# Kernel optimization log

Hardware: AMD Instinct MI355X
Metric: run time of the kernel (lower is better)

The kernel has to match this reference:

```python
import jax, jax.numpy as jnp
import numpy as np

X_DIM, Y_DIM = 16, 8
D_MODEL, N_HEADS, N_LAYERS = 256, 8, 8
D_HEAD = D_MODEL // N_HEADS            # 32 (hidden_out_size // n_heads)
D_FF = D_HEAD * 8 * N_HEADS            # 2048 (feed_forward_dimensions)
B, S_PAST, S_FUT = 4, 1024, 512
MIN_STD = 0.01
LN_EPS = 1e-5
ATTN_EPS = 1e-6


def setup_inputs() -> dict:
    key = jax.random.key(0)
    ks = jax.random.split(key, 24)
    def nrm(k, shape, s=0.02):
        return jax.random.normal(k, shape, jnp.float32) * s
    L, d, dff = N_LAYERS, D_MODEL, D_FF
    x_size = X_DIM + Y_DIM
    return {
        "past_x": jax.random.normal(ks[0], (B, S_PAST, X_DIM), jnp.float32),
        "past_y": jax.random.normal(ks[1], (B, S_PAST, Y_DIM), jnp.float32),
        "future_x": jax.random.normal(ks[2], (B, S_FUT, X_DIM), jnp.float32),
        "enc_W": nrm(ks[3], (x_size, d)), "enc_b": jnp.zeros((d,), jnp.float32),
        "Wq": nrm(ks[4], (L, d, d)), "bq": jnp.zeros((L, d), jnp.float32),
        "Wk": nrm(ks[5], (L, d, d)), "bk": jnp.zeros((L, d), jnp.float32),
        "Wv": nrm(ks[6], (L, d, d)), "bv": jnp.zeros((L, d), jnp.float32),
        "Wo": nrm(ks[7], (L, d, d)), "bo": jnp.zeros((L, d), jnp.float32),
        "ln1_w": jnp.ones((L, d), jnp.float32), "ln1_b": jnp.zeros((L, d), jnp.float32),
        "W1": nrm(ks[8], (L, d, dff)), "b1": jnp.zeros((L, dff), jnp.float32),
        "W2": nrm(ks[9], (L, dff, d)), "b2": jnp.zeros((L, d), jnp.float32),
        "ln2_w": jnp.ones((L, d), jnp.float32), "ln2_b": jnp.zeros((L, d), jnp.float32),
        "mean_W": nrm(ks[10], (d, Y_DIM)), "mean_b": jnp.zeros((Y_DIM,), jnp.float32),
        "std_W": nrm(ks[11], (d, Y_DIM)), "std_b": jnp.zeros((Y_DIM,), jnp.float32),
    }


def _ln(x, w, b):
    m = jnp.mean(x, axis=-1, keepdims=True)
    v = jnp.var(x, axis=-1, keepdims=True)
    return (x - m) * jax.lax.rsqrt(v + LN_EPS) * w + b


def _causal_linear_attn(q, k, v):
    # q,k,v: [B, N, H, D]; phi(x) = elu(x) + 1 (fast_transformers default feature map)
    q = jax.nn.elu(q) + 1.0
    k = jax.nn.elu(k) + 1.0
    # cumulative outer-product state S_i = sum_{j<=i} phi(k_j) v_j^T : [B,N,H,D,D]
    kv = jnp.cumsum(jnp.einsum('bnhd,bnhm->bnhdm', k, v), axis=1)
    num = jnp.einsum('bnhd,bnhdm->bnhm', q, kv)
    z = jnp.einsum('bnhd,bnhd->bnh', q, jnp.cumsum(k, axis=1))
    return num / (z[..., None] + ATTN_EPS)


def _forward(past_x, past_y, future_x, enc_W, enc_b, Wq, bq, Wk, bk, Wv, bv,
             Wo, bo, ln1_w, ln1_b, W1, b1, W2, b2, ln2_w, ln2_b,
             mean_W, mean_b, std_W, std_b):
    Bz, Sf = future_x.shape[0], future_x.shape[1]
    steps = past_y.shape[1]
    # future y placeholder = last observed y, repeated
    fy = jnp.repeat(past_y[:, -1:, :], Sf, axis=1)
    context = jnp.concatenate([past_x, past_y], axis=-1)
    target = jnp.concatenate([future_x, fy], axis=-1)
    x = jax.lax.stop_gradient(jnp.concatenate([context, target], axis=1))  # .detach()
    x = x @ enc_W + enc_b                      # [B, N, D_MODEL]
    N = x.shape[1]
    for i in range(N_LAYERS):
        q = (x @ Wq[i] + bq[i]).reshape(Bz, N, N_HEADS, D_HEAD)
        k = (x @ Wk[i] + bk[i]).reshape(Bz, N, N_HEADS, D_HEAD)
        v = (x @ Wv[i] + bv[i]).reshape(Bz, N, N_HEADS, D_HEAD)
        a = _causal_linear_attn(q, k, v).reshape(Bz, N, D_MODEL)
        x = _ln(x + (a @ Wo[i] + bo[i]), ln1_w[i], ln1_b[i])   # post-norm (fast_transformers)
        y = jax.nn.relu(x @ W1[i] + b1[i]) @ W2[i] + b2[i]
        x = _ln(x + y, ln2_w[i], ln2_b[i])
    out = x[:, steps:, :]                      # keep only the target segment
    mean = out @ mean_W + mean_b
    sigma = MIN_STD + (1.0 - MIN_STD) * jax.nn.softplus(out @ std_W + std_b)
    return mean, sigma


def reference(past_x, past_y, future_x, enc_W, enc_b, Wq, bq, Wk, bk, Wv, bv,
              Wo, bo, ln1_w, ln1_b, W1, b1, W2, b2, ln2_w, ln2_b,
              mean_W, mean_b, std_W, std_b):
    return _forward(past_x, past_y, future_x, enc_W, enc_b, Wq, bq, Wk, bk,
                    Wv, bv, Wo, bo, ln1_w, ln1_b, W1, b1, W2, b2,
                    ln2_w, ln2_b, mean_W, mean_b, std_W, std_b)
```

## Files before the change

kernel.cpp:

```cpp
#include <hip/hip_runtime.h>
#include <hip/hip_bf16.h>
#include <math.h>

#define BB 4
#define SP 1024
#define SF 512
#define NN 1536
#define DD 256
#define HH 8
#define DH 32
#define DFF 2048
#define LL 8
#define TOK (BB*NN)
#define NSEG 48
#define SEGLEN 32

typedef __attribute__((ext_vector_type(8))) short bf16x8;
typedef __attribute__((ext_vector_type(4))) float f32x4;
typedef __hip_bfloat16 bf16;

__device__ __forceinline__ void gld_lds16(const void* g, void* l) {
    __builtin_amdgcn_global_load_lds(
        (const __attribute__((address_space(1))) void*)g,
        (__attribute__((address_space(3))) void*)l, 16, 0, 0);
}

__device__ __forceinline__ unsigned short f2bf_u(float f) {
    return __builtin_bit_cast(unsigned short, __float2bfloat16(f));
}

__device__ __forceinline__ void wtrans_tile(
    const float* __restrict__ s, bf16* __restrict__ d, int K, int N,
    int k0, int n0)
{
    __shared__ float tile[64][65];
    int t = threadIdx.x, c = t & 63, r4 = t >> 6;
    #pragma unroll
    for (int rr = 0; rr < 64; rr += 4)
        tile[rr+r4][c] = s[(size_t)(k0+rr+r4)*N + n0 + c];
    __syncthreads();
    #pragma unroll
    for (int rr = 0; rr < 64; rr += 4) {
        int n = rr + r4;
        d[(size_t)(n0+n)*K + k0 + c] = __float2bfloat16(tile[c][n]);
    }
}

__global__ __launch_bounds__(256) void wtrans_kernel(
    const float* __restrict__ src, bf16* __restrict__ dst, int K, int N)
{
    wtrans_tile(src + (size_t)blockIdx.z*K*N, dst + (size_t)blockIdx.z*K*N,
                K, N, blockIdx.x*64, blockIdx.y*64);
}

__global__ __launch_bounds__(256) void wtrans4_kernel(
    const float* __restrict__ Wq, const float* __restrict__ Wk,
    const float* __restrict__ Wv, const float* __restrict__ Wo,
    bf16* __restrict__ Wqt, bf16* __restrict__ Wkt,
    bf16* __restrict__ Wvt, bf16* __restrict__ Wot)
{
    int z = blockIdx.z, which = z >> 3, l = z & 7;
    const float* s = (which == 0 ? Wq : which == 1 ? Wk : which == 2 ? Wv : Wo)
                     + (size_t)l*DD*DD;
    bf16* d = (which == 0 ? Wqt : which == 1 ? Wkt : which == 2 ? Wvt : Wot)
              + (size_t)l*DD*DD;
    wtrans_tile(s, d, DD, DD, blockIdx.x*64, blockIdx.y*64);
}

template<int BM, bool SLICE, bool BOUT>
__device__ __forceinline__ void gemm_core(
    const bf16* __restrict__ A, const bf16* __restrict__ Wt,
    const float* __restrict__ bias, float* __restrict__ Cf,
    bf16* __restrict__ Cb, int N, int K, int epi, int kc0, int kc1)
{
    constexpr int MI = BM/32;
    __shared__ bf16 As[BM*64];
    __shared__ bf16 Bs[128*64];
    int tid = threadIdx.x, lane = tid & 63, wid = tid >> 6;
    int m0 = blockIdx.x*BM, n0 = blockIdx.y*128;
    int wm = (wid & 1)*(BM/2), wn = (wid >> 1)*64;

    f32x4 acc[MI][4] = {};

    int rA = wid*(BM/4) + (lane >> 3);
    int rB = wid*32 + (lane >> 3);
    int c_st = (lane & 7)*8;
    const bf16* Ag = A  + (size_t)(m0 + rA)*K + c_st;
    const bf16* Bg = Wt + (size_t)(n0 + rB)*K + c_st;
    bf16* Asw = As + (wid*(BM/4))*64;
    bf16* Bsw = Bs + (wid*32)*64;

    int a_off = (wm + (lane & 15))*64 + (lane >> 4)*8;
    int b_off = (wn + (lane & 15))*64 + (lane >> 4)*8;

    for (int kc = kc0; kc < kc1; kc += 64) {
        #pragma unroll
        for (int i = 0; i < MI; i++)
            gld_lds16(Ag + (size_t)(i*8)*K + kc, Asw + (i*8)*64);
        #pragma unroll
        for (int i = 0; i < 4; i++)
            gld_lds16(Bg + (size_t)(i*8)*K + kc, Bsw + (i*8)*64);
        __syncthreads();
        #pragma unroll
        for (int ks = 0; ks < 2; ks++) {
            bf16x8 af[MI], bfr[4];
            #pragma unroll
            for (int i = 0; i < MI; i++)
                af[i] = *(const bf16x8*)(As + a_off + i*16*64 + ks*32);
            #pragma unroll
            for (int j = 0; j < 4; j++)
                bfr[j] = *(const bf16x8*)(Bs + b_off + j*16*64 + ks*32);
            #pragma unroll
            for (int i = 0; i < MI; i++)
                #pragma unroll
                for (int j = 0; j < 4; j++)
                    acc[i][j] = __builtin_amdgcn_mfma_f32_16x16x32_bf16(
                        af[i], bfr[j], acc[i][j], 0, 0, 0);
        }
        __syncthreads();
    }

    if constexpr (BOUT) {
        bf16* Ct = Bs;
        #pragma unroll
        for (int j = 0; j < 4; j++) {
            int col = wn + j*16 + (lane & 15);
            float bv = bias[n0 + col];
            #pragma unroll
            for (int i = 0; i < MI; i++) {
                #pragma unroll
                for (int r = 0; r < 4; r++) {
                    int row = wm + i*16 + (lane >> 4)*4 + r;
                    float v = acc[i][j][r] + bv;
                    if (epi == 1) v = fmaxf(v, 0.f);
                    else if (epi == 2) v = (v > 0.f) ? v + 1.f : expf(v);
                    Ct[row*128 + (col ^ (((row >> 2) & 3) << 4))] = __float2bfloat16(v);
                }
            }
        }
        __syncthreads();
        #pragma unroll
        for (int u = 0; u < 4; u++) {
            int e = tid*32 + u*8;
            int row = e >> 7, c0 = e & 127;
            bf16x8 val = *(const bf16x8*)(Ct + row*128 + (c0 ^ (((row >> 2) & 3) << 4)));
            *(bf16x8*)(Cb + (size_t)(m0 + row)*N + n0 + c0) = val;
        }
    } else {
        int col_base = n0 + wn + (lane & 15);
        int row_base = m0 + wm + (lane >> 4)*4;
        #pragma unroll
        for (int j = 0; j < 4; j++) {
            int col = col_base + j*16;
            float bv = SLICE ? 0.f : bias[col];
            #pragma unroll
            for (int i = 0; i < MI; i++) {
                #pragma unroll
                for (int r = 0; r < 4; r++) {
                    int row = row_base + i*16 + r;
                    if (SLICE) {
                        Cf[(size_t)row*N + col] = acc[i][j][r];
                    } else {
                        float v = acc[i][j][r] + bv;
                        if (epi == 1) v = fmaxf(v, 0.f);
                        else if (epi == 2) v = (v > 0.f) ? v + 1.f : expf(v);
                        if (Cb) Cb[(size_t)row*N + col] = __float2bfloat16(v);
                        else    Cf[(size_t)row*N + col] = v;
                    }
                }
            }
        }
    }
}

template<int BM, bool BOUT>
__global__ __launch_bounds__(256) void mfma_gemm_kernel(
    const bf16* __restrict__ A, const bf16* __restrict__ Wt,
    const float* __restrict__ bias, float* __restrict__ Cf,
    bf16* __restrict__ Cb, int N, int K, int epi)
{
    gemm_core<BM, false, BOUT>(A, Wt, bias, Cf, Cb, N, K, epi, 0, K);
}

template<int BM>
__global__ __launch_bounds__(256) void mfma_gemm_slicek_kernel(
    const bf16* __restrict__ A, const bf16* __restrict__ Wt,
    float* __restrict__ Cf, int N, int K, int KC)
{
    int kc0 = blockIdx.z*KC;
    gemm_core<BM, true, false>(A, Wt, nullptr, Cf + (size_t)blockIdx.z*TOK*N,
                               nullptr, N, K, 0, kc0, kc0 + KC);
}

template<int BM>
__global__ __launch_bounds__(256) void mfma_qkv_kernel(
    const bf16* __restrict__ Xb,
    const bf16* __restrict__ Wqt, const bf16* __restrict__ Wkt, const bf16* __restrict__ Wvt,
    const float* __restrict__ bq, const float* __restrict__ bk, const float* __restrict__ bv,
    float* __restrict__ Q, float* __restrict__ K, float* __restrict__ V, int layer)
{
    int z = blockIdx.z;
    const bf16* Wt = (z == 0) ? Wqt : (z == 1) ? Wkt : Wvt;
    const float* b = (z == 0) ? bq : (z == 1) ? bk : bv;
    float* C = (z == 0) ? Q : (z == 1) ? K : V;
    gemm_core<BM, false, false>(Xb, Wt + (size_t)layer*DD*DD, b + (size_t)layer*DD,
                                C, nullptr, DD, DD, (z == 2) ? 0 : 2, 0, DD);
}

__global__ __launch_bounds__(256) void wo_ln_kernel(
    const bf16* __restrict__ A, const bf16* __restrict__ Wt,
    const float* __restrict__ bias,
    const float* __restrict__ lnw, const float* __restrict__ lnb,
    float* __restrict__ X, bf16* __restrict__ Xb)
{
    __shared__ bf16 As[32*64];
    __shared__ bf16 Bs[256*64];
    __shared__ float red[2][4][32];
    int tid = threadIdx.x, lane = tid & 63, wid = tid >> 6;
    int m0 = blockIdx.x*32;
    int wn = wid*64;

    f32x4 acc[2][4] = {};

    int rA = wid*8 + (lane >> 3);
    int c_st = (lane & 7)*8;
    const bf16* Ag = A + (size_t)(m0 + rA)*DD + c_st;
    const bf16* Bg = Wt + (size_t)(wn + (lane >> 3))*DD + c_st;
    bf16* Asw = As + (wid*8)*64;
    bf16* Bsw = Bs + wn*64;

    int a_off = (lane & 15)*64 + (lane >> 4)*8;
    int b_off = (wn + (lane & 15))*64 + (lane >> 4)*8;

    for (int kc = 0; kc < DD; kc += 64) {
        gld_lds16(Ag + kc, Asw);
        #pragma unroll
        for (int i = 0; i < 8; i++)
            gld_lds16(Bg + (size_t)(i*8)*DD + kc, Bsw + (i*8)*64);
        __syncthreads();
        #pragma unroll
        for (int ks = 0; ks < 2; ks++) {
            bf16x8 af[2], bfr[4];
            af[0] = *(const bf16x8*)(As + a_off + ks*32);
            af[1] = *(const bf16x8*)(As + a_off + 16*64 + ks*32);
            #pragma unroll
            for (int j = 0; j < 4; j++)
                bfr[j] = *(const bf16x8*)(Bs + b_off + j*16*64 + ks*32);
            #pragma unroll
            for (int i = 0; i < 2; i++)
                #pragma unroll
                for (int j = 0; j < 4; j++)
                    acc[i][j] = __builtin_amdgcn_mfma_f32_16x16x32_bf16(
                        af[i], bfr[j], acc[i][j], 0, 0, 0);
        }
        __syncthreads();
    }

    #pragma unroll
    for (int j = 0; j < 4; j++) {
        int c = wn + j*16 + (lane & 15);
        float bv = bias[c];
        #pragma unroll
        for (int i = 0; i < 2; i++) {
            int row = m0 + i*16 + (lane >> 4)*4;
            #pragma unroll
            for (int r = 0; r < 4; r++)
                acc[i][j][r] += bv + X[(size_t)(row + r)*DD + c];
        }
    }
    #pragma unroll
    for (int i = 0; i < 2; i++) {
        #pragma unroll
        for (int r = 0; r < 4; r++) {
            float s  = (acc[i][0][r] + acc[i][1][r]) + (acc[i][2][r] + acc[i][3][r]);
            float s2 = (acc[i][0][r]*acc[i][0][r] + acc[i][1][r]*acc[i][1][r])
                     + (acc[i][2][r]*acc[i][2][r] + acc[i][3][r]*acc[i][3][r]);
            #pragma unroll
            for (int off = 1; off < 16; off <<= 1) {
                s  += __shfl_xor(s,  off, 64);
                s2 += __shfl_xor(s2, off, 64);
            }
            if ((lane & 15) == 0) {
                int rloc = i*16 + (lane >> 4)*4 + r;
                red[0][wid][rloc] = s;
                red[1][wid][rloc] = s2;
            }
        }
    }
    __syncthreads();
    #pragma unroll
    for (int i = 0; i < 2; i++) {
        #pragma unroll
        for (int r = 0; r < 4; r++) {
            int rloc = i*16 + (lane >> 4)*4 + r;
            float S  = (red[0][0][rloc] + red[0][1][rloc]) + (red[0][2][rloc] + red[0][3][rloc]);
            float S2 = (red[1][0][rloc] + red[1][1][rloc]) + (red[1][2][rloc] + red[1][3][rloc]);
            float mean = S * (1.f/256.f);
            float var  = S2 * (1.f/256.f) - mean*mean;
            float rs = rsqrtf(var + 1e-5f);
            #pragma unroll
            for (int j = 0; j < 4; j++) {
                int c = wn + j*16 + (lane & 15);
                float o = (acc[i][j][r] - mean) * rs * lnw[c] + lnb[c];
                size_t idx = (size_t)(m0 + rloc)*DD + c;
                X[idx] = o;
                Xb[idx] = __float2bfloat16(o);
            }
        }
    }
}

__global__ __launch_bounds__(256) void encode_kernel(
    const float* __restrict__ px, const float* __restrict__ py,
    const float* __restrict__ fx, const float* __restrict__ encW,
    const float* __restrict__ encb, float* __restrict__ X, bf16* __restrict__ Xb)
{
    int tok = blockIdx.x;
    int t = threadIdx.x;
    int b = tok / NN, n = tok % NN;
    __shared__ float in[24];
    if (t < 16) {
        in[t] = (n < SP) ? px[((size_t)b*SP + n)*16 + t]
                         : fx[((size_t)b*SF + (n - SP))*16 + t];
    } else if (t < 24) {
        int j = t - 16;
        in[t] = (n < SP) ? py[((size_t)b*SP + n)*8 + j]
                         : py[((size_t)b*SP + (SP-1))*8 + j];
    }
    __syncthreads();
    float acc = encb[t];
    #pragma unroll
    for (int j = 0; j < 24; j++) acc = fmaf(in[j], encW[j*DD + t], acc);
    X[(size_t)tok*DD + t] = acc;
    Xb[(size_t)tok*DD + t] = __float2bfloat16(acc);
}

__global__ __launch_bounds__(256) void attnA_kernel(
    const float* __restrict__ K, const float* __restrict__ V,
    float* __restrict__ SegS, float* __restrict__ SegZ)
{
    int bid = blockIdx.x;
    int seg = bid % NSEG; int bh = bid / NSEG;
    int h = bh & 7, b = bh >> 3;
    int t = threadIdx.x;
    int d = t & 31, mg = t >> 5, m0 = mg*4;
    int tok0 = b*NN + seg*SEGLEN;
    const float* Kp = K + (size_t)tok0*DD + h*DH;
    const float* Vp = V + (size_t)tok0*DD + h*DH;
    float a0=0,a1=0,a2=0,a3=0, ks=0;
    #pragma unroll 4
    for (int i = 0; i < SEGLEN; i++) {
        float kd = Kp[(size_t)i*DD + d];
        float4 vv = *(const float4*)(Vp + (size_t)i*DD + m0);
        a0 = fmaf(kd, vv.x, a0); a1 = fmaf(kd, vv.y, a1);
        a2 = fmaf(kd, vv.z, a2); a3 = fmaf(kd, vv.w, a3);
        ks += kd;
    }
    float4 o = {a0, a1, a2, a3};
    *(float4*)(SegS + ((size_t)bid*32 + d)*32 + m0) = o;
    if (mg == 0) SegZ[(size_t)bid*32 + d] = ks;
}

__global__ __launch_bounds__(256) void attnA2_kernel(
    float* __restrict__ SegS, float* __restrict__ SegZ)
{
    int bh = blockIdx.x, y = blockIdx.y, t = threadIdx.x;
    int e = y*256 + t;
    float* p = SegS + (size_t)bh*NSEG*1024 + e;
    float v[NSEG];
    #pragma unroll
    for (int s = 0; s < NSEG; s++) v[s] = p[(size_t)s*1024];
    float run = 0.f;
    #pragma unroll
    for (int s = 0; s < NSEG; s++) {
        p[(size_t)s*1024] = run;
        run += v[s];
    }
    if (y == 0 && t < 32) {
        float* pz = SegZ + (size_t)bh*NSEG*32 + t;
        float vz[NSEG];
        #pragma unroll
        for (int s = 0; s < NSEG; s++) vz[s] = pz[(size_t)s*32];
        float runz = 0.f;
        #pragma unroll
        for (int s = 0; s < NSEG; s++) {
            pz[(size_t)s*32] = runz;
            runz += vz[s];
        }
    }
}

__global__ __launch_bounds__(256) void attnB_kernel(
    const float* __restrict__ Q, const float* __restrict__ K, const float* __restrict__ V,
    const float* __restrict__ SegS, const float* __restrict__ SegZ,
    bf16* __restrict__ A)
{
    int wid = threadIdx.x >> 6;
    int lane = threadIdx.x & 63;
    int bid = blockIdx.x*4 + wid;
    int seg = bid % NSEG; int bh = bid / NSEG;
    int h = bh & 7, b = bh >> 3;
    int m = lane & 31, dh = lane >> 5, dh16 = dh*16;
    int tok0 = b*NN + seg*SEGLEN;

    __shared__ float qs[4][SEGLEN][32], ksm[4][SEGLEN][32], vs[4][SEGLEN][32];
    const float* Qp = Q + (size_t)tok0*DD + h*DH;
    const float* Kp = K + (size_t)tok0*DD + h*DH;
    const float* Vp = V + (size_t)tok0*DD + h*DH;
    #pragma unroll
    for (int f = lane; f < SEGLEN*8; f += 64) {
        int r = f >> 3, c = (f & 7)*4;
        *(float4*)&qs[wid][r][c]  = *(const float4*)(Qp + (size_t)r*DD + c);
        *(float4*)&ksm[wid][r][c] = *(const float4*)(Kp + (size_t)r*DD + c);
        *(float4*)&vs[wid][r][c]  = *(const float4*)(Vp + (size_t)r*DD + c);
    }
    __syncthreads();

    float kv[16], kss[16];
    const float* Pp = SegS + (size_t)bid*1024;
    const float* Zp = SegZ + (size_t)bid*32;
    #pragma unroll
    for (int j = 0; j < 16; j++) {
        kv[j]  = Pp[(dh16 + j)*32 + m];
        kss[j] = Zp[dh16 + j];
    }

    bf16* Ap = A + (size_t)tok0*DD + h*DH;
    for (int i = 0; i < SEGLEN; i++) {
        float qv[16], kk[16];
        #pragma unroll
        for (int c = 0; c < 4; c++) {
            float4 t4 = *(const float4*)&qs[wid][i][dh16 + 4*c];
            qv[4*c] = t4.x; qv[4*c+1] = t4.y; qv[4*c+2] = t4.z; qv[4*c+3] = t4.w;
            float4 k4 = *(const float4*)&ksm[wid][i][dh16 + 4*c];
            kk[4*c] = k4.x; kk[4*c+1] = k4.y; kk[4*c+2] = k4.z; kk[4*c+3] = k4.w;
        }
        float vm = vs[wid][i][m];
        #pragma unroll
        for (int j = 0; j < 16; j++) {
            kv[j] = fmaf(kk[j], vm, kv[j]);
            kss[j] += kk[j];
        }
        float p0=0,p1=0,p2=0,p3=0,z0=0,z1=0,z2=0,z3=0;
        #pragma unroll
        for (int j = 0; j < 4; j++) {
            p0 = fmaf(qv[j],     kv[j],     p0);
            p1 = fmaf(qv[4+j],   kv[4+j],   p1);
            p2 = fmaf(qv[8+j],   kv[8+j],   p2);
            p3 = fmaf(qv[12+j],  kv[12+j],  p3);
            z0 = fmaf(qv[j],     kss[j],    z0);
            z1 = fmaf(qv[4+j],   kss[4+j],  z1);
            z2 = fmaf(qv[8+j],   kss[8+j],  z2);
            z3 = fmaf(qv[12+j],  kss[12+j], z3);
        }
        float nump = (p0+p1)+(p2+p3);
        float zp   = (z0+z1)+(z2+z3);
        nump += __shfl_xor(nump, 32, 64);
        zp   += __shfl_xor(zp,   32, 64);
        if (dh == 0) Ap[(size_t)i*DD + m] = __float2bfloat16(nump / (zp + 1e-6f));
    }
}

__global__ __launch_bounds__(256) void resid_ln2_kernel(
    const float* __restrict__ Xin, const float* __restrict__ G2,
    const float* __restrict__ gb,
    const float* __restrict__ w, const float* __restrict__ b,
    float* __restrict__ Xout, bf16* __restrict__ Xbout)
{
    const size_t SZ = (size_t)TOK*DD;
    int wid = threadIdx.x >> 6, lane = threadIdx.x & 63;
    int tok = blockIdx.x*4 + wid;
    int c0 = lane*4;
    size_t idx = (size_t)tok*DD + c0;
    float4 xi = *(const float4*)(Xin + idx);
    float4 g0 = *(const float4*)(G2 + idx);
    float4 g1 = *(const float4*)(G2 + SZ + idx);
    float4 gbv = *(const float4*)(gb + c0);
    float v0 = xi.x + gbv.x + g0.x + g1.x;
    float v1 = xi.y + gbv.y + g0.y + g1.y;
    float v2 = xi.z + gbv.z + g0.z + g1.z;
    float v3 = xi.w + gbv.w + g0.w + g1.w;
    float s  = (v0 + v1) + (v2 + v3);
    float s2 = (v0*v0 + v1*v1) + (v2*v2 + v3*v3);
    #pragma unroll
    for (int off = 32; off >= 1; off >>= 1) {
        s  += __shfl_xor(s,  off, 64);
        s2 += __shfl_xor(s2, off, 64);
    }
    float mean = s * (1.f/256.f);
    float var  = s2 * (1.f/256.f) - mean*mean;
    float rs = rsqrtf(var + 1e-5f);
    float4 wv = *(const float4*)(w + c0);
    float4 bv = *(const float4*)(b + c0);
    float o0 = (v0 - mean) * rs * wv.x + bv.x;
    float o1 = (v1 - mean) * rs * wv.y + bv.y;
    float o2 = (v2 - mean) * rs * wv.z + bv.z;
    float o3 = (v3 - mean) * rs * wv.w + bv.w;
    float4 o = {o0, o1, o2, o3};
    *(float4*)(Xout + idx) = o;
    ushort4 ob = {f2bf_u(o0), f2bf_u(o1), f2bf_u(o2), f2bf_u(o3)};
    *(ushort4*)((unsigned short*)Xbout + idx) = ob;
}

__global__ __launch_bounds__(256) void head_kernel(
    const float* __restrict__ X,
    const float* __restrict__ meanW, const float* __restrict__ meanB,
    const float* __restrict__ stdW,  const float* __restrict__ stdB,
    float* __restrict__ out)
{
    int wv = threadIdx.x >> 6;
    int lane = threadIdx.x & 63;
    int idx = blockIdx.x*4 + wv;
    int b = idx / SF, i = idx % SF;
    const float* row = X + ((size_t)(b*NN + SP + i))*DD;
    __shared__ float xs[4][DD];
    *(float4*)&xs[wv][lane*4] = *(const float4*)(row + lane*4);
    __syncthreads();

    int j = lane & 7;
    int which = (lane >> 3) & 1;
    int seg = lane >> 4;
    const float* W = which ? stdW : meanW;
    float p = 0.f;
    #pragma unroll 16
    for (int d = seg*64; d < seg*64 + 64; d++) p = fmaf(xs[wv][d], W[d*8 + j], p);
    p += __shfl_xor(p, 16, 64);
    p += __shfl_xor(p, 32, 64);
    if (lane < 16) {
        if (which == 0) {
            out[((size_t)b*SF + i)*8 + j] = p + meanB[j];
        } else {
            float s = p + stdB[j];
            float sp = fmaxf(s, 0.f) + log1pf(expf(-fabsf(s)));
            out[(size_t)BB*SF*8 + ((size_t)b*SF + i)*8 + j] = 0.01f + 0.99f*sp;
        }
    }
}

extern "C" void kernel_launch(void* const* d_in, const int* in_sizes, int n_in,
                              void* d_out, int out_size, void* d_ws, size_t ws_size,
                              hipStream_t stream)
{
    (void)in_sizes; (void)n_in; (void)out_size; (void)ws_size;
    const float* past_x   = (const float*)d_in[0];
    const float* past_y   = (const float*)d_in[1];
    const float* future_x = (const float*)d_in[2];
    const float* enc_W    = (const float*)d_in[3];
    const float* enc_b    = (const float*)d_in[4];
    const float* Wq       = (const float*)d_in[5];
    const float* bq       = (const float*)d_in[6];
    const float* Wk       = (const float*)d_in[7];
    const float* bk       = (const float*)d_in[8];
    const float* Wv       = (const float*)d_in[9];
    const float* bv       = (const float*)d_in[10];
    const float* Wo       = (const float*)d_in[11];
    const float* bo       = (const float*)d_in[12];
    const float* ln1_w    = (const float*)d_in[13];
    const float* ln1_b    = (const float*)d_in[14];
    const float* W1       = (const float*)d_in[15];
    const float* b1       = (const float*)d_in[16];
    const float* W2       = (const float*)d_in[17];
    const float* b2       = (const float*)d_in[18];
    const float* ln2_w    = (const float*)d_in[19];
    const float* ln2_b    = (const float*)d_in[20];
    const float* mean_W   = (const float*)d_in[21];
    const float* mean_b   = (const float*)d_in[22];
    const float* std_W    = (const float*)d_in[23];
    const float* std_b    = (const float*)d_in[24];
    float* out = (float*)d_out;

    char* base = (char*)d_ws;
    size_t off = 0;
    float* X  = (float*)(base + off); off += (size_t)TOK*DD*4;
    bf16* Xb  = (bf16*)(base + off);  off += (size_t)TOK*DD*2;
    bf16* Hb  = (bf16*)(base + off);  off += (size_t)TOK*DFF*2;
    float* Qb = (float*)Hb;
    float* Kb = Qb + (size_t)TOK*DD;
    float* Vb = Kb + (size_t)TOK*DD;
    bf16* Ab  = (bf16*)(base + off);  off += (size_t)TOK*DD*2;
    float* G2 = (float*)(base + off); off += (size_t)2*TOK*DD*4;
    float* SegS = (float*)(base + off); off += (size_t)BB*HH*NSEG*1024*4;
    float* SegZ = (float*)(base + off); off += (size_t)BB*HH*NSEG*32*4;
    bf16* Wqt = (bf16*)(base + off); off += (size_t)LL*DD*DD*2;
    bf16* Wkt = (bf16*)(base + off); off += (size_t)LL*DD*DD*2;
    bf16* Wvt = (bf16*)(base + off); off += (size_t)LL*DD*DD*2;
    bf16* Wot = (bf16*)(base + off); off += (size_t)LL*DD*DD*2;
    bf16* W1t = (bf16*)(base + off); off += (size_t)LL*DD*DFF*2;
    bf16* W2t = (bf16*)(base + off); off += (size_t)LL*DFF*DD*2;

    wtrans4_kernel<<<dim3(4, 4, 4*LL), 256, 0, stream>>>(
        Wq, Wk, Wv, Wo, Wqt, Wkt, Wvt, Wot);
    wtrans_kernel<<<dim3(4, 32, LL), 256, 0, stream>>>(W1, W1t, DD, DFF);
    wtrans_kernel<<<dim3(32, 4, LL), 256, 0, stream>>>(W2, W2t, DFF, DD);

    encode_kernel<<<TOK, 256, 0, stream>>>(past_x, past_y, future_x, enc_W, enc_b, X, Xb);

    for (int l = 0; l < LL; l++) {
        mfma_qkv_kernel<32><<<dim3(TOK/32, 2, 3), 256, 0, stream>>>(
            Xb, Wqt, Wkt, Wvt, bq, bk, bv, Qb, Kb, Vb, l);
        attnA_kernel<<<BB*HH*NSEG, 256, 0, stream>>>(Kb, Vb, SegS, SegZ);
        attnA2_kernel<<<dim3(BB*HH, 4), 256, 0, stream>>>(SegS, SegZ);
        attnB_kernel<<<BB*HH*NSEG/4, 256, 0, stream>>>(Qb, Kb, Vb, SegS, SegZ, Ab);
        wo_ln_kernel<<<TOK/32, 256, 0, stream>>>(
            Ab, Wot + (size_t)l*DD*DD, bo + (size_t)l*DD,
            ln1_w + l*DD, ln1_b + l*DD, X, Xb);
        mfma_gemm_kernel<64, true><<<dim3(TOK/64, DFF/128), 256, 0, stream>>>(
            Xb, W1t + (size_t)l*DD*DFF, b1 + (size_t)l*DFF, nullptr, Hb, DFF, DD, 1);
        mfma_gemm_slicek_kernel<32><<<dim3(TOK/32, 2, 2), 256, 0, stream>>>(
            Hb, W2t + (size_t)l*DFF*DD, G2, DD, DFF, DFF/2);
        resid_ln2_kernel<<<TOK/4, 256, 0, stream>>>(
            X, G2, b2 + (size_t)l*DD, ln2_w + l*DD, ln2_b + l*DD, X, Xb);
    }

    head_kernel<<<(BB*SF)/4, 256, 0, stream>>>(X, mean_W, mean_b, std_W, std_b, out);
}
```

Before: 1.004 ms.

## Fuse segment prefix scan and residual LayerNorm via last-block atomic counters

Removes the separate attnA2 prefix-scan kernel and the resid_ln2 kernel by having the last block to finish, detected with an atomic counter and threadfence, do the follow-up work inside attnA and the split-K W2 GEMM. Counters are zeroed with one memset per forward call, and each layer uses its own slice. This cuts 16 kernel launches and the gaps between them. In exchange, the scan for each (batch, head) and the LN for each row tile are done serially by a single block, which can lengthen the tail of each kernel.

```diff
diff --git a/kernel.cpp b/kernel.cpp
--- a/kernel.cpp
+++ b/kernel.cpp
@@ -183,16 +183,6 @@
 }
 
 template<int BM>
-__global__ __launch_bounds__(256) void mfma_gemm_slicek_kernel(
-    const bf16* __restrict__ A, const bf16* __restrict__ Wt,
-    float* __restrict__ Cf, int N, int K, int KC)
-{
-    int kc0 = blockIdx.z*KC;
-    gemm_core<BM, true, false>(A, Wt, nullptr, Cf + (size_t)blockIdx.z*TOK*N,
-                               nullptr, N, K, 0, kc0, kc0 + KC);
-}
-
-template<int BM>
 __global__ __launch_bounds__(256) void mfma_qkv_kernel(
     const bf16* __restrict__ Xb,
     const bf16* __restrict__ Wqt, const bf16* __restrict__ Wkt, const bf16* __restrict__ Wvt,
@@ -205,6 +195,61 @@
     float* C = (z == 0) ? Q : (z == 1) ? K : V;
     gemm_core<BM, false, false>(Xb, Wt + (size_t)layer*DD*DD, b + (size_t)layer*DD,
                                 C, nullptr, DD, DD, (z == 2) ? 0 : 2, 0, DD);
+}
+
+__global__ __launch_bounds__(256) void w2_ln_kernel(
+    const bf16* __restrict__ A, const bf16* __restrict__ Wt,
+    float* __restrict__ G2,
+    const float* __restrict__ gb, const float* __restrict__ lnw,
+    const float* __restrict__ lnb,
+    float* __restrict__ X, bf16* __restrict__ Xb, unsigned* __restrict__ ctr)
+{
+    int z = blockIdx.z;
+    int kc0 = z*(DFF/2);
+    gemm_core<32, true, false>(A, Wt, nullptr, G2 + (size_t)z*TOK*DD, nullptr,
+                               DD, DFF, 0, kc0, kc0 + DFF/2);
+    __threadfence();
+    __shared__ unsigned done;
+    if (threadIdx.x == 0) done = atomicAdd(&ctr[blockIdx.x], 1u);
+    __syncthreads();
+    if (done != 3u) return;
+    __threadfence();
+
+    const size_t SZ = (size_t)TOK*DD;
+    int m0 = blockIdx.x*32;
+    int wid = threadIdx.x >> 6, lane = threadIdx.x & 63;
+    int c0 = lane*4;
+    float4 gbv = *(const float4*)(gb + c0);
+    float4 wv  = *(const float4*)(lnw + c0);
+    float4 bv  = *(const float4*)(lnb + c0);
+    for (int rr = wid; rr < 32; rr += 4) {
+        size_t idx = (size_t)(m0 + rr)*DD + c0;
+        float4 xi = *(const float4*)(X + idx);
+        float4 g0 = *(const float4*)(G2 + idx);
+        float4 g1 = *(const float4*)(G2 + SZ + idx);
+        float v0 = xi.x + gbv.x + g0.x + g1.x;
+        float v1 = xi.y + gbv.y + g0.y + g1.y;
+        float v2 = xi.z + gbv.z + g0.z + g1.z;
+        float v3 = xi.w + gbv.w + g0.w + g1.w;
+        float s  = (v0 + v1) + (v2 + v3);
+        float s2 = (v0*v0 + v1*v1) + (v2*v2 + v3*v3);
+        #pragma unroll
+        for (int off = 32; off >= 1; off >>= 1) {
+            s  += __shfl_xor(s,  off, 64);
+            s2 += __shfl_xor(s2, off, 64);
+        }
+        float mean = s * (1.f/256.f);
+        float var  = s2 * (1.f/256.f) - mean*mean;
+        float rs = rsqrtf(var + 1e-5f);
+        float o0 = (v0 - mean) * rs * wv.x + bv.x;
+        float o1 = (v1 - mean) * rs * wv.y + bv.y;
+        float o2 = (v2 - mean) * rs * wv.z + bv.z;
+        float o3 = (v3 - mean) * rs * wv.w + bv.w;
+        float4 o = {o0, o1, o2, o3};
+        *(float4*)(X + idx) = o;
+        ushort4 ob = {f2bf_u(o0), f2bf_u(o1), f2bf_u(o2), f2bf_u(o3)};
+        *(ushort4*)((unsigned short*)Xb + idx) = ob;
+    }
 }
 
 __global__ __launch_bounds__(256) void wo_ln_kernel(
@@ -337,7 +382,8 @@
 
 __global__ __launch_bounds__(256) void attnA_kernel(
     const float* __restrict__ K, const float* __restrict__ V,
-    float* __restrict__ SegS, float* __restrict__ SegZ)
+    float* __restrict__ SegS, float* __restrict__ SegZ,
+    unsigned* __restrict__ ctr)
 {
     int bid = blockIdx.x;
     int seg = bid % NSEG; int bh = bid / NSEG;
@@ -359,34 +405,33 @@
     float4 o = {a0, a1, a2, a3};
     *(float4*)(SegS + ((size_t)bid*32 + d)*32 + m0) = o;
     if (mg == 0) SegZ[(size_t)bid*32 + d] = ks;
-}
-
-__global__ __launch_bounds__(256) void attnA2_kernel(
-    float* __restrict__ SegS, float* __restrict__ SegZ)
-{
-    int bh = blockIdx.x, y = blockIdx.y, t = threadIdx.x;
-    int e = y*256 + t;
-    float* p = SegS + (size_t)bh*NSEG*1024 + e;
-    float v[NSEG];
-    #pragma unroll
-    for (int s = 0; s < NSEG; s++) v[s] = p[(size_t)s*1024];
-    float run = 0.f;
-    #pragma unroll
-    for (int s = 0; s < NSEG; s++) {
-        p[(size_t)s*1024] = run;
-        run += v[s];
-    }
-    if (y == 0 && t < 32) {
+
+    __threadfence();
+    __shared__ unsigned done;
+    if (t == 0) done = atomicAdd(&ctr[bh], 1u);
+    __syncthreads();
+    if (done != NSEG - 1) return;
+    __threadfence();
+
+    float* baseS = SegS + (size_t)bh*NSEG*1024;
+    #pragma unroll 1
+    for (int y = 0; y < 4; y++) {
+        float* p = baseS + y*256 + t;
+        float v[NSEG];
+        #pragma unroll
+        for (int s = 0; s < NSEG; s++) v[s] = p[(size_t)s*1024];
+        float run = 0.f;
+        #pragma unroll
+        for (int s = 0; s < NSEG; s++) { p[(size_t)s*1024] = run; run += v[s]; }
+    }
+    if (t < 32) {
         float* pz = SegZ + (size_t)bh*NSEG*32 + t;
         float vz[NSEG];
         #pragma unroll
         for (int s = 0; s < NSEG; s++) vz[s] = pz[(size_t)s*32];
         float runz = 0.f;
         #pragma unroll
-        for (int s = 0; s < NSEG; s++) {
-            pz[(size_t)s*32] = runz;
-            runz += vz[s];
-        }
+        for (int s = 0; s < NSEG; s++) { pz[(size_t)s*32] = runz; runz += vz[s]; }
     }
 }
 
@@ -459,47 +504,6 @@
         zp   += __shfl_xor(zp,   32, 64);
         if (dh == 0) Ap[(size_t)i*DD + m] = __float2bfloat16(nump / (zp + 1e-6f));
     }
-}
-
-__global__ __launch_bounds__(256) void resid_ln2_kernel(
-    const float* __restrict__ Xin, const float* __restrict__ G2,
-    const float* __restrict__ gb,
-    const float* __restrict__ w, const float* __restrict__ b,
-    float* __restrict__ Xout, bf16* __restrict__ Xbout)
-{
-    const size_t SZ = (size_t)TOK*DD;
-    int wid = threadIdx.x >> 6, lane = threadIdx.x & 63;
-    int tok = blockIdx.x*4 + wid;
-    int c0 = lane*4;
-    size_t idx = (size_t)tok*DD + c0;
-    float4 xi = *(const float4*)(Xin + idx);
-    float4 g0 = *(const float4*)(G2 + idx);
-    float4 g1 = *(const float4*)(G2 + SZ + idx);
-    float4 gbv = *(const float4*)(gb + c0);
-    float v0 = xi.x + gbv.x + g0.x + g1.x;
-    float v1 = xi.y + gbv.y + g0.y + g1.y;
-    float v2 = xi.z + gbv.z + g0.z + g1.z;
-    float v3 = xi.w + gbv.w + g0.w + g1.w;
-    float s  = (v0 + v1) + (v2 + v3);
-    float s2 = (v0*v0 + v1*v1) + (v2*v2 + v3*v3);
-    #pragma unroll
-    for (int off = 32; off >= 1; off >>= 1) {
-        s  += __shfl_xor(s,  off, 64);
-        s2 += __shfl_xor(s2, off, 64);
-    }
-    float mean = s * (1.f/256.f);
-    float var  = s2 * (1.f/256.f) - mean*mean;
-    float rs = rsqrtf(var + 1e-5f);
-    float4 wv = *(const float4*)(w + c0);
-    float4 bv = *(const float4*)(b + c0);
-    float o0 = (v0 - mean) * rs * wv.x + bv.x;
-    float o1 = (v1 - mean) * rs * wv.y + bv.y;
-    float o2 = (v2 - mean) * rs * wv.z + bv.z;
-    float o3 = (v3 - mean) * rs * wv.w + bv.w;
-    float4 o = {o0, o1, o2, o3};
-    *(float4*)(Xout + idx) = o;
-    ushort4 ob = {f2bf_u(o0), f2bf_u(o1), f2bf_u(o2), f2bf_u(o3)};
-    *(ushort4*)((unsigned short*)Xbout + idx) = ob;
 }
 
 __global__ __launch_bounds__(256) void head_kernel(
@@ -587,6 +591,10 @@
     bf16* Wot = (bf16*)(base + off); off += (size_t)LL*DD*DD*2;
     bf16* W1t = (bf16*)(base + off); off += (size_t)LL*DD*DFF*2;
     bf16* W2t = (bf16*)(base + off); off += (size_t)LL*DFF*DD*2;
+    unsigned* CtrA = (unsigned*)(base + off); off += (size_t)LL*BB*HH*4;
+    unsigned* CtrW = (unsigned*)(base + off); off += (size_t)LL*(TOK/32)*4;
+
+    hipMemsetAsync(CtrA, 0, (size_t)(LL*BB*HH + LL*(TOK/32))*4, stream);
 
     wtrans4_kernel<<<dim3(4, 4, 4*LL), 256, 0, stream>>>(
         Wq, Wk, Wv, Wo, Wqt, Wkt, Wvt, Wot);
@@ -598,18 +606,18 @@
     for (int l = 0; l < LL; l++) {
         mfma_qkv_kernel<32><<<dim3(TOK/32, 2, 3), 256, 0, stream>>>(
             Xb, Wqt, Wkt, Wvt, bq, bk, bv, Qb, Kb, Vb, l);
-        attnA_kernel<<<BB*HH*NSEG, 256, 0, stream>>>(Kb, Vb, SegS, SegZ);
-        attnA2_kernel<<<dim3(BB*HH, 4), 256, 0, stream>>>(SegS, SegZ);
+        attnA_kernel<<<BB*HH*NSEG, 256, 0, stream>>>(
+            Kb, Vb, SegS, SegZ, CtrA + l*BB*HH);
         attnB_kernel<<<BB*HH*NSEG/4, 256, 0, stream>>>(Qb, Kb, Vb, SegS, SegZ, Ab);
         wo_ln_kernel<<<TOK/32, 256, 0, stream>>>(
             Ab, Wot + (size_t)l*DD*DD, bo + (size_t)l*DD,
             ln1_w + l*DD, ln1_b + l*DD, X, Xb);
         mfma_gemm_kernel<64, true><<<dim3(TOK/64, DFF/128), 256, 0, stream>>>(
             Xb, W1t + (size_t)l*DD*DFF, b1 + (size_t)l*DFF, nullptr, Hb, DFF, DD, 1);
-        mfma_gemm_slicek_kernel<32><<<dim3(TOK/32, 2, 2), 256, 0, stream>>>(
-            Hb, W2t + (size_t)l*DFF*DD, G2, DD, DFF, DFF/2);
-        resid_ln2_kernel<<<TOK/4, 256, 0, stream>>>(
-            X, G2, b2 + (size_t)l*DD, ln2_w + l*DD, ln2_b + l*DD, X, Xb);
+        w2_ln_kernel<<<dim3(TOK/32, 2, 2), 256, 0, stream>>>(
+            Hb, W2t + (size_t)l*DFF*DD, G2,
+            b2 + (size_t)l*DD, ln2_w + l*DD, ln2_b + l*DD,
+            X, Xb, CtrW + l*(TOK/32));
     }
 
     head_kernel<<<(BB*SF)/4, 256, 0, stream>>>(X, mean_W, mean_b, std_W, std_b, out);
```

Result: slower. 3.608 ms (+259.4%).
